# Kernel tuning notes

Measured on AMD Instinct MI355X. Metric: run time of the kernel, lower is better.

Reference implementation:

```python
import jax, jax.numpy as jnp
import numpy as np

MAX_LENGTH = 11
SOS_TOKEN = 0
H = 256      # hidden_dim
V = 32000    # output_dim (vocab)
B = 256      # batch
S = 64       # encoder seq len


def setup_inputs() -> dict:
    key = jax.random.key(0)
    ks = jax.random.split(key, 16)
    sc = 0.05
    return {
        "encoder_outputs": jax.random.normal(ks[0], (B, S, H), jnp.float32),
        "encoder_hidden": jax.random.normal(ks[1], (1, B, H), jnp.float32),
        "target_tensor": jax.random.randint(ks[2], (B, MAX_LENGTH), 0, V),
        "embedding": jax.random.normal(ks[3], (V, H), jnp.float32) * sc,
        "Wa": jax.random.normal(ks[4], (H, H), jnp.float32) * sc,
        "ba": jnp.zeros((H,), jnp.float32),
        "Ua": jax.random.normal(ks[5], (H, H), jnp.float32) * sc,
        "bua": jnp.zeros((H,), jnp.float32),
        "Va": jax.random.normal(ks[6], (H, 1), jnp.float32) * sc,
        "bva": jnp.zeros((1,), jnp.float32),
        "W_ih": jax.random.normal(ks[7], (H, 2 * H), jnp.float32) * sc,
        "b_ih": jnp.zeros((H,), jnp.float32),
        "W_hh": jax.random.normal(ks[8], (H, H), jnp.float32) * sc,
        "b_hh": jnp.zeros((H,), jnp.float32),
        "W_out": jax.random.normal(ks[9], (V, H), jnp.float32) * sc,
        "b_out": jnp.zeros((V,), jnp.float32),
    }


def _decode(encoder_outputs, encoder_hidden, target_tensor,
            embedding, Wa, ba, Ua, bua, Va, bva,
            W_ih, b_ih, W_hh, b_hh, W_out, b_out):
    batch = encoder_outputs.shape[0]
    # Ua(keys) is step-invariant: precompute once.  [B, S, H]
    uk = jnp.einsum('bsh,kh->bsk', encoder_outputs, Ua) + bua
    h0 = encoder_hidden[0]  # [B, H]
    # teacher forcing: input at step i is SOS for i=0, else target[:, i-1]
    tokens = jnp.concatenate(
        [jnp.full((batch, 1), SOS_TOKEN, dtype=target_tensor.dtype),
         target_tensor[:, :MAX_LENGTH - 1]], axis=1)  # [B, T]

    def step(h, tok):
        emb = embedding[tok]                                   # [B, H]
        q = jnp.einsum('bh,kh->bk', h, Wa) + ba                # Wa(query)
        scores = jnp.tanh(q[:, None, :] + uk) @ Va + bva       # [B, S, 1]
        attn = jax.nn.softmax(scores[..., 0], axis=-1)         # [B, S]
        ctx = jnp.einsum('bs,bsh->bh', attn, encoder_outputs)  # [B, H]
        x = jnp.concatenate([emb, ctx], axis=-1)               # [B, 2H]
        h_new = jnp.tanh(x @ W_ih.T + b_ih + h @ W_hh.T + b_hh)
        logits = h_new @ W_out.T + b_out                       # [B, V]
        return h_new, (logits, attn)

    h_last, (logits, attns) = jax.lax.scan(step, h0, tokens.T)
    decoder_outputs = jax.nn.log_softmax(
        jnp.transpose(logits, (1, 0, 2)), axis=-1)             # [B, T, V]
    attentions = jnp.transpose(attns, (1, 0, 2))               # [B, T, S]
    return decoder_outputs, h_last[None], attentions


def reference(encoder_outputs, encoder_hidden, target_tensor,
              embedding, Wa, ba, Ua, bua, Va, bva,
              W_ih, b_ih, W_hh, b_hh, W_out, b_out):
    return _decode(encoder_outputs, encoder_hidden, target_tensor,
                   embedding, Wa, ba, Ua, bua, Va, bva,
                   W_ih, b_ih, W_hh, b_hh, W_out, b_out)
```

## Files before the change

kernel.cpp:

```cpp
#include <hip/hip_runtime.h>

#define Bz 256
#define Sz 64
#define Hz 256
#define Vz 32000
#define Tz 11
#define Mz (Bz*Tz)

typedef __attribute__((ext_vector_type(8))) short bf16x8;
typedef __attribute__((ext_vector_type(4))) float f32x4;

__device__ __forceinline__ float blo(unsigned int u){ return __builtin_bit_cast(float, u<<16); }
__device__ __forceinline__ float bhi(unsigned int u){ return __builtin_bit_cast(float, u & 0xffff0000u); }
__device__ __forceinline__ unsigned short f2bf(float f){
  unsigned int x = __builtin_bit_cast(unsigned int, f);
  return (unsigned short)((x + 0x7fffu + ((x>>16)&1u)) >> 16);
}
__device__ __forceinline__ float bf2f(unsigned short u){ return __builtin_bit_cast(float, ((unsigned int)u)<<16); }
__device__ __forceinline__ float ftanh(float x){ float e = __expf(2.f*x); return 1.f - 2.f/(e+1.f); }

__device__ __forceinline__ float dot8(uint4 wv, const float* base){
  float4 h0 = *(const float4*)(base);
  float4 h1 = *(const float4*)(base+4);
  return blo(wv.x)*h0.x + bhi(wv.x)*h0.y + blo(wv.y)*h0.z + bhi(wv.y)*h0.w
       + blo(wv.z)*h1.x + bhi(wv.z)*h1.y + blo(wv.w)*h1.z + bhi(wv.w)*h1.w;
}

__device__ __forceinline__ void gll16(const unsigned short* g, unsigned short* l){
  __builtin_amdgcn_global_load_lds(
      (const __attribute__((address_space(1))) unsigned int*)g,
      (__attribute__((address_space(3))) unsigned int*)l, 16, 0, 0);
}

__global__ __launch_bounds__(256) void k_prep(
    const float* __restrict__ Wa,
    const float* __restrict__ Wih, const float* __restrict__ Whh,
    const int* __restrict__ target, const float* __restrict__ embedding,
    const float* __restrict__ b_ih,
    const float* __restrict__ enc, const float* __restrict__ Ua,
    const float* __restrict__ bua,
    unsigned short* __restrict__ wa_p,
    unsigned short* __restrict__ wih2_p, unsigned short* __restrict__ whh_p,
    float* __restrict__ E, unsigned short* __restrict__ uk_b){
  __shared__ float rows[16][Hz];
  int tid = threadIdx.x;
  int bid = blockIdx.x;
  if (bid < 256){
    int i = bid*256 + tid;
    int k = i>>8, j = i&255;
    int p = ((j>>3)*256 + k)*8 + (j&7);
    wa_p[p]   = f2bf(Wa[i]);
    whh_p[p]  = f2bf(Whh[i]);
    wih2_p[p] = f2bf(Wih[k*512 + 256 + j]);
  } else if (bid < 256+176){
    int m0 = (bid-256)*16;
    for (int r=0;r<16;r++){
      int m = m0 + r; int b = m/11, t = m - b*11;
      int tok = (t==0) ? 0 : target[b*11 + (t-1)];
      rows[r][tid] = embedding[(size_t)tok*Hz + tid];
    }
    __syncthreads();
    float acc[16];
    #pragma unroll
    for (int r=0;r<16;r++) acc[r]=0.f;
    const float* wrow = Wih + tid*512;
    for (int j4=0;j4<64;j4++){
      float4 w = *(const float4*)(wrow + j4*4);
      #pragma unroll
      for (int r=0;r<16;r++){
        float4 e = *(const float4*)(&rows[r][j4*4]);
        acc[r] += w.x*e.x + w.y*e.y + w.z*e.z + w.w*e.w;
      }
    }
    float bi = b_ih[tid];
    for (int r=0;r<16;r++) E[(m0+r)*Hz + tid] = acc[r] + bi;
  } else {
    int r0 = (bid-(256+176))*16;
    for (int r=0;r<16;r++) rows[r][tid] = enc[(size_t)(r0+r)*Hz + tid];
    __syncthreads();
    float acc[16];
    #pragma unroll
    for (int r=0;r<16;r++) acc[r]=0.f;
    const float* wrow = Ua + tid*Hz;
    for (int j4=0;j4<64;j4++){
      float4 w = *(const float4*)(wrow + j4*4);
      #pragma unroll
      for (int r=0;r<16;r++){
        float4 e = *(const float4*)(&rows[r][j4*4]);
        acc[r] += w.x*e.x + w.y*e.y + w.z*e.z + w.w*e.w;
      }
    }
    float bk = bua[tid];
    for (int r=0;r<16;r++) uk_b[(size_t)(r0+r)*Hz + tid] = f2bf(acc[r] + bk);
  }
}

__global__ __launch_bounds__(512) __attribute__((amdgpu_waves_per_eu(2,4)))
void k_rnn(
    const float* __restrict__ enc, const float* __restrict__ ench,
    const float* __restrict__ ba, const float* __restrict__ Va,
    const float* __restrict__ bva, const float* __restrict__ b_hh,
    const unsigned short* __restrict__ uk_b, const unsigned short* __restrict__ wa_p,
    const unsigned short* __restrict__ wih2_p, const unsigned short* __restrict__ whh_p,
    const float* __restrict__ E, unsigned short* __restrict__ hs_b,
    float* __restrict__ out_hlast, float* __restrict__ out_attn,
    const float* __restrict__ Wout, unsigned short* __restrict__ wout_b){
  __shared__ __align__(16) unsigned short uk_lds[Sz][Hz];
  __shared__ __align__(16) unsigned short enc_lds[Sz][Hz];
  __shared__ __align__(16) float h_lds[Hz];
  __shared__ __align__(16) float ctx_lds[Hz];
  __shared__ __align__(16) float redq[2][Hz];
  __shared__ __align__(16) float redh_a[2][Hz];
  __shared__ __align__(16) float redh[2][Hz];
  __shared__ float sc_lds[Sz];
  __shared__ float attn_lds[Sz];
  int tid = threadIdx.x;

  if (blockIdx.x >= Bz){
    int i = (blockIdx.x - Bz)*512 + tid;
    const int stride = 1024*512;
    for (int idx = i; idx < Vz*Hz; idx += stride) wout_b[idx] = f2bf(Wout[idx]);
    return;
  }

  int b = blockIdx.x;
  int k = tid & 255, qd = tid >> 8;
  int lane = tid & 63, wv = tid >> 6;
  const int rot = (b & 3) << 2;

  {
    const uint4* src = (const uint4*)(uk_b + (size_t)b*Sz*Hz);
    uint4* dst = (uint4*)(&uk_lds[0][0]);
    #pragma unroll
    for (int i=0;i<4;i++) dst[i*512+tid] = src[i*512+tid];
  }
  {
    const float4* src = (const float4*)(enc + (size_t)b*Sz*Hz);
    #pragma unroll
    for (int i=0;i<8;i++){
      int idx = i*512 + tid;
      float4 v = src[idx];
      ushort4 p; p.x=f2bf(v.x); p.y=f2bf(v.y); p.z=f2bf(v.z); p.w=f2bf(v.w);
      *(ushort4*)((unsigned short*)(&enc_lds[0][0]) + idx*4) = p;
    }
  }
  if (tid < Hz) h_lds[tid] = ench[b*Hz + tid];
  float va_r[4], ba4[4];
  #pragma unroll
  for (int c=0;c<4;c++){ va_r[c] = Va[lane + 64*c]; ba4[c] = ba[lane + 64*c]; }
  float bhh_k = b_hh[k], bva_s = bva[0];

  const uint4* wap = (const uint4*)(wa_p)   + (size_t)qd*16*256 + k;
  const uint4* whp = (const uint4*)(whh_p)  + (size_t)qd*16*256 + k;
  const uint4* w2p = (const uint4*)(wih2_p) + (size_t)qd*16*256 + k;
  __syncthreads();

  for (int t=0; t<Tz; t++){
    int m = b*Tz + t;
    const float* hb = &h_lds[qd*128];
    {
      float a0=0.f, a1=0.f, a2=0.f, a3=0.f;
      #pragma unroll 2
      for (int jx=0;jx<16;jx+=4){
        int jj = (jx + rot) & 15;
        uint4 w0=wap[(jj+0)*256], w1=wap[(jj+1)*256], w2=wap[(jj+2)*256], w3=wap[(jj+3)*256];
        a0 += dot8(w0, hb + jj*8 +  0);
        a1 += dot8(w1, hb + jj*8 +  8);
        a2 += dot8(w2, hb + jj*8 + 16);
        a3 += dot8(w3, hb + jj*8 + 24);
      }
      redq[qd][k] = (a0+a1) + (a2+a3);
      float b0=0.f, b1=0.f, b2=0.f, b3=0.f;
      #pragma unroll 2
      for (int jx=0;jx<16;jx+=4){
        int jj = (jx + rot) & 15;
        uint4 w0=whp[(jj+0)*256], w1=whp[(jj+1)*256], w2=whp[(jj+2)*256], w3=whp[(jj+3)*256];
        b0 += dot8(w0, hb + jj*8 +  0);
        b1 += dot8(w1, hb + jj*8 +  8);
        b2 += dot8(w2, hb + jj*8 + 16);
        b3 += dot8(w3, hb + jj*8 + 24);
      }
      redh_a[qd][k] = (b0+b1) + (b2+b3);
    }
    float e_pre = E[(size_t)m*Hz + k];
    __syncthreads();
    {
      float ql[4];
      #pragma unroll
      for (int c=0;c<4;c++){
        int p = lane + 64*c;
        ql[c] = redq[0][p] + redq[1][p] + ba4[c];
      }
      #pragma unroll
      for (int si=0; si<8; si++){
        int s = wv*8 + si;
        float p = 0.f;
        #pragma unroll
        for (int c=0;c<4;c++){
          float u = bf2f(uk_lds[s][lane + 64*c]);
          p += ftanh(ql[c] + u) * va_r[c];
        }
        #pragma unroll
        for (int off=1; off<64; off<<=1) p += __shfl_xor(p, off, 64);
        if (lane==0) sc_lds[s] = p + bva_s;
      }
    }
    __syncthreads();
    {
      float sv = sc_lds[lane];
      float mx = sv;
      #pragma unroll
      for (int off=1; off<64; off<<=1) mx = fmaxf(mx, __shfl_xor(mx, off, 64));
      float e = __expf(sv - mx);
      float sum = e;
      #pragma unroll
      for (int off=1; off<64; off<<=1) sum += __shfl_xor(sum, off, 64);
      float a = e / sum;
      if (wv == 0){
        attn_lds[lane] = a;
        out_attn[(size_t)m*Sz + lane] = a;
      }
    }
    __syncthreads();
    {
      float c0=0.f, c1=0.f;
      #pragma unroll
      for (int i=0;i<32;i+=2){
        int s = qd*32 + i;
        c0 += attn_lds[s]   * bf2f(enc_lds[s][k]);
        c1 += attn_lds[s+1] * bf2f(enc_lds[s+1][k]);
      }
      redq[qd][k] = c0 + c1;
    }
    __syncthreads();
    if (qd == 0) ctx_lds[k] = redq[0][k] + redq[1][k];
    __syncthreads();
    {
      const float* cb = &ctx_lds[qd*128];
      float a0=0.f, a1=0.f, a2=0.f, a3=0.f;
      #pragma unroll 2
      for (int jx=0;jx<16;jx+=4){
        int jj = (jx + rot) & 15;
        uint4 w0=w2p[(jj+0)*256], w1=w2p[(jj+1)*256], w2=w2p[(jj+2)*256], w3=w2p[(jj+3)*256];
        a0 += dot8(w0, cb + jj*8 +  0);
        a1 += dot8(w1, cb + jj*8 +  8);
        a2 += dot8(w2, cb + jj*8 + 16);
        a3 += dot8(w3, cb + jj*8 + 24);
      }
      redh[qd][k] = (a0+a1) + (a2+a3);
    }
    __syncthreads();
    if (qd == 0){
      float acc = e_pre + bhh_k
                + redh_a[0][k] + redh_a[1][k]
                + redh[0][k]   + redh[1][k];
      float hn = ftanh(acc);
      h_lds[k] = hn;
      hs_b[(size_t)m*Hz + k] = f2bf(hn);
      if (t==Tz-1) out_hlast[b*Hz + k] = hn;
    }
    __syncthreads();
  }
}

__global__ __launch_bounds__(256, 4) void k_gemm(
    const unsigned short* __restrict__ Ab, const unsigned short* __restrict__ Bb,
    const float* __restrict__ b_out, const float* __restrict__ lse,
    float* __restrict__ out, float* __restrict__ partials){
  __shared__ __align__(16) unsigned short As[128*64];
  __shared__ __align__(16) unsigned short Bs[128*64];
  int tid = threadIdx.x;
  int fid = blockIdx.x;
  int xcd = fid & 7, wu = fid >> 3;
  int wid = (xcd < 4 ? xcd*688 : 4*688 + (xcd-4)*687) + wu;
  int bn = wid / 22;
  int bm = wid - bn*22;
  int m0 = bm*128, n0 = bn*128;
  int w = tid>>6, lane = tid&63;
  int wm = w>>1, wn = w&1;
  f32x4 acc[4][4];
  #pragma unroll
  for (int i=0;i<4;i++)
    #pragma unroll
    for (int j=0;j<4;j++) acc[i][j] = (f32x4){0.f,0.f,0.f,0.f};

  for (int ktx=0; ktx<4; ktx++){
    int kt = (ktx + bm) & 3;
    __syncthreads();
    #pragma unroll
    for (int i=0;i<4;i++){
      int chunk = i*256 + tid;
      int row = chunk>>3, c8 = chunk&7;
      gll16(Ab + (size_t)(m0+row)*Hz + kt*64 + c8*8, &As[(i*256 + w*64)*8]);
      gll16(Bb + (size_t)(n0+row)*Hz + kt*64 + c8*8, &Bs[(i*256 + w*64)*8]);
    }
    __syncthreads();
    #pragma unroll
    for (int ks=0; ks<2; ks++){
      bf16x8 af[4], bg[4];
      #pragma unroll
      for (int i=0;i<4;i++){
        int row = wm*64 + i*16 + (lane&15);
        af[i] = *(const bf16x8*)(&As[row*64 + ks*32 + (lane>>4)*8]);
      }
      #pragma unroll
      for (int j=0;j<4;j++){
        int row = wn*64 + j*16 + (lane&15);
        bg[j] = *(const bf16x8*)(&Bs[row*64 + ks*32 + (lane>>4)*8]);
      }
      #pragma unroll
      for (int i=0;i<4;i++)
        #pragma unroll
        for (int j=0;j<4;j++)
          acc[i][j] = __builtin_amdgcn_mfma_f32_16x16x32_bf16(af[i], bg[j], acc[i][j], 0,0,0);
    }
  }
  int col_l = lane & 15, rgrp = lane >> 4;
  float bj[4];
  #pragma unroll
  for (int j=0;j<4;j++) bj[j] = b_out[n0 + wn*64 + j*16 + col_l];
  if (lse == nullptr){
    #pragma unroll
    for (int i=0;i<4;i++){
      int rowbase = m0 + wm*64 + i*16 + rgrp*4;
      #pragma unroll
      for (int r=0;r<4;r++){
        float se = 0.f;
        #pragma unroll
        for (int j=0;j<4;j++) se += __expf(acc[i][j][r] + bj[j]);
        se += __shfl_xor(se,1,64); se += __shfl_xor(se,2,64);
        se += __shfl_xor(se,4,64); se += __shfl_xor(se,8,64);
        if (col_l == 0) partials[(size_t)(bn*2+wn)*Mz + rowbase + r] = se;
      }
    }
  } else {
    #pragma unroll
    for (int i=0;i<4;i++){
      int rowbase = m0 + wm*64 + i*16 + rgrp*4;
      #pragma unroll
      for (int r=0;r<4;r++){
        float l = lse[rowbase + r];
        #pragma unroll
        for (int j=0;j<4;j++){
          int col = n0 + wn*64 + j*16 + col_l;
          out[(size_t)(rowbase+r)*Vz + col] = acc[i][j][r] + bj[j] - l;
        }
      }
    }
  }
}

__global__ __launch_bounds__(256) void k_lse(const float* __restrict__ partials,
                                             float* __restrict__ lse){
  int m = blockIdx.x*256 + threadIdx.x;
  if (m < Mz){
    float s = 0.f;
    for (int c=0;c<500;c++) s += partials[(size_t)c*Mz + m];
    lse[m] = logf(s);
  }
}

extern "C" void kernel_launch(void* const* d_in, const int* in_sizes, int n_in,
                              void* d_out, int out_size, void* d_ws, size_t ws_size,
                              hipStream_t stream) {
  const float* enc   = (const float*)d_in[0];
  const float* ench  = (const float*)d_in[1];
  const int*   target= (const int*)d_in[2];
  const float* emb   = (const float*)d_in[3];
  const float* Wa    = (const float*)d_in[4];
  const float* ba    = (const float*)d_in[5];
  const float* Ua    = (const float*)d_in[6];
  const float* bua   = (const float*)d_in[7];
  const float* Va    = (const float*)d_in[8];
  const float* bva   = (const float*)d_in[9];
  const float* Wih   = (const float*)d_in[10];
  const float* bih   = (const float*)d_in[11];
  const float* Whh   = (const float*)d_in[12];
  const float* bhh   = (const float*)d_in[13];
  const float* Wout  = (const float*)d_in[14];
  const float* bout  = (const float*)d_in[15];

  float* out = (float*)d_out;
  float* out_logits = out;
  float* out_hlast  = out + (size_t)Mz*Vz;
  float* out_attn   = out_hlast + Bz*Hz;

  char* ws = (char*)d_ws;
  unsigned short* wout_b = (unsigned short*)(ws);
  unsigned short* wa_p   = (unsigned short*)(ws + 16384000);
  unsigned short* wih2_p = (unsigned short*)(ws + 16515072);
  unsigned short* whh_p  = (unsigned short*)(ws + 16646144);
  unsigned short* hs_b   = (unsigned short*)(ws + 16777216);
  float*          lse    = (float*)(ws + 18219008);

  char* sc = (char*)d_out;
  unsigned short* uk_b     = (unsigned short*)(sc);
  float*          E        = (float*)(sc + 8388608);
  float*          partials = (float*)(sc + 11272192);

  k_prep <<<256+176+1024, 256, 0, stream>>>(Wa, Wih, Whh,
                                            target, emb, bih, enc, Ua, bua,
                                            wa_p, wih2_p, whh_p, E, uk_b);
  k_rnn  <<<Bz+1024, 512, 0, stream>>>(enc, ench, ba, Va, bva, bhh,
                                       uk_b, wa_p, wih2_p, whh_p, E, hs_b,
                                       out_hlast, out_attn, Wout, wout_b);
  k_gemm <<<5500, 256, 0, stream>>>(hs_b, wout_b, bout, nullptr, out_logits, partials);
  k_lse  <<<11, 256, 0, stream>>>(partials, lse);
  k_gemm <<<5500, 256, 0, stream>>>(hs_b, wout_b, bout, lse, out_logits, partials);
}
```

Baseline: 372.2 us.

## Split RNN step work across three thread groups and parallelize LSE reduction

The recurrent kernel now uses 768 threads per batch row instead of 512. The K dimension of the Wa/Whh/Wih matvecs and the context reduction are split three ways, with per-block rotation of the segment assignment, to shorten the per-step serial chain. The LSE kernel now has 8 threads cooperate per row via shuffles instead of one thread looping over 500 partials. The trade-offs are uneven segment lengths, extra reduction terms, and higher register and occupancy pressure from the larger block.

```diff
diff --git a/kernel.cpp b/kernel.cpp
--- a/kernel.cpp
+++ b/kernel.cpp
@@ -95,7 +95,7 @@
   }
 }
 
-__global__ __launch_bounds__(512) __attribute__((amdgpu_waves_per_eu(2,4)))
+__global__ __launch_bounds__(768) __attribute__((amdgpu_waves_per_eu(3,6)))
 void k_rnn(
     const float* __restrict__ enc, const float* __restrict__ ench,
     const float* __restrict__ ba, const float* __restrict__ Va,
@@ -109,16 +109,16 @@
   __shared__ __align__(16) unsigned short enc_lds[Sz][Hz];
   __shared__ __align__(16) float h_lds[Hz];
   __shared__ __align__(16) float ctx_lds[Hz];
-  __shared__ __align__(16) float redq[2][Hz];
-  __shared__ __align__(16) float redh_a[2][Hz];
-  __shared__ __align__(16) float redh[2][Hz];
+  __shared__ __align__(16) float redq[3][Hz];
+  __shared__ __align__(16) float redh_a[3][Hz];
+  __shared__ __align__(16) float redh[3][Hz];
   __shared__ float sc_lds[Sz];
   __shared__ float attn_lds[Sz];
   int tid = threadIdx.x;
 
   if (blockIdx.x >= Bz){
-    int i = (blockIdx.x - Bz)*512 + tid;
-    const int stride = 1024*512;
+    int i = (blockIdx.x - Bz)*768 + tid;
+    const int stride = 1024*768;
     for (int idx = i; idx < Vz*Hz; idx += stride) wout_b[idx] = f2bf(Wout[idx]);
     return;
   }
@@ -126,22 +126,28 @@
   int b = blockIdx.x;
   int k = tid & 255, qd = tid >> 8;
   int lane = tid & 63, wv = tid >> 6;
-  const int rot = (b & 3) << 2;
+  int qe = qd + (b % 3); if (qe >= 3) qe -= 3;
+  const int jst = (qe==0) ? 0 : (qe==1) ? 11 : 22;
+  const int jlen = (qe==2) ? 10 : 11;
+  const int dst_ = (qe==0) ? 0 : (qe==1) ? 22 : 43;
+  const int dlen = (qe==0) ? 22 : 21;
 
   {
     const uint4* src = (const uint4*)(uk_b + (size_t)b*Sz*Hz);
     uint4* dst = (uint4*)(&uk_lds[0][0]);
     #pragma unroll
-    for (int i=0;i<4;i++) dst[i*512+tid] = src[i*512+tid];
+    for (int i=0;i<3;i++){ int idx = i*768 + tid; if (idx < 2048) dst[idx] = src[idx]; }
   }
   {
     const float4* src = (const float4*)(enc + (size_t)b*Sz*Hz);
     #pragma unroll
-    for (int i=0;i<8;i++){
-      int idx = i*512 + tid;
-      float4 v = src[idx];
-      ushort4 p; p.x=f2bf(v.x); p.y=f2bf(v.y); p.z=f2bf(v.z); p.w=f2bf(v.w);
-      *(ushort4*)((unsigned short*)(&enc_lds[0][0]) + idx*4) = p;
+    for (int i=0;i<6;i++){
+      int idx = i*768 + tid;
+      if (idx < 4096){
+        float4 v = src[idx];
+        ushort4 p; p.x=f2bf(v.x); p.y=f2bf(v.y); p.z=f2bf(v.z); p.w=f2bf(v.w);
+        *(ushort4*)((unsigned short*)(&enc_lds[0][0]) + idx*4) = p;
+      }
     }
   }
   if (tid < Hz) h_lds[tid] = ench[b*Hz + tid];
@@ -150,37 +156,32 @@
   for (int c=0;c<4;c++){ va_r[c] = Va[lane + 64*c]; ba4[c] = ba[lane + 64*c]; }
   float bhh_k = b_hh[k], bva_s = bva[0];
 
-  const uint4* wap = (const uint4*)(wa_p)   + (size_t)qd*16*256 + k;
-  const uint4* whp = (const uint4*)(whh_p)  + (size_t)qd*16*256 + k;
-  const uint4* w2p = (const uint4*)(wih2_p) + (size_t)qd*16*256 + k;
+  const uint4* wap = (const uint4*)(wa_p)   + k;
+  const uint4* whp = (const uint4*)(whh_p)  + k;
+  const uint4* w2p = (const uint4*)(wih2_p) + k;
   __syncthreads();
 
   for (int t=0; t<Tz; t++){
     int m = b*Tz + t;
-    const float* hb = &h_lds[qd*128];
     {
-      float a0=0.f, a1=0.f, a2=0.f, a3=0.f;
-      #pragma unroll 2
-      for (int jx=0;jx<16;jx+=4){
-        int jj = (jx + rot) & 15;
-        uint4 w0=wap[(jj+0)*256], w1=wap[(jj+1)*256], w2=wap[(jj+2)*256], w3=wap[(jj+3)*256];
-        a0 += dot8(w0, hb + jj*8 +  0);
-        a1 += dot8(w1, hb + jj*8 +  8);
-        a2 += dot8(w2, hb + jj*8 + 16);
-        a3 += dot8(w3, hb + jj*8 + 24);
-      }
-      redq[qd][k] = (a0+a1) + (a2+a3);
-      float b0=0.f, b1=0.f, b2=0.f, b3=0.f;
-      #pragma unroll 2
-      for (int jx=0;jx<16;jx+=4){
-        int jj = (jx + rot) & 15;
-        uint4 w0=whp[(jj+0)*256], w1=whp[(jj+1)*256], w2=whp[(jj+2)*256], w3=whp[(jj+3)*256];
-        b0 += dot8(w0, hb + jj*8 +  0);
-        b1 += dot8(w1, hb + jj*8 +  8);
-        b2 += dot8(w2, hb + jj*8 + 16);
-        b3 += dot8(w3, hb + jj*8 + 24);
-      }
-      redh_a[qd][k] = (b0+b1) + (b2+b3);
+      float a0=0.f, a1=0.f;
+      for (int jx=0; jx+1<jlen; jx+=2){
+        int jj = jst + jx;
+        uint4 w0 = wap[jj*256], w1 = wap[(jj+1)*256];
+        a0 += dot8(w0, &h_lds[jj*8]);
+        a1 += dot8(w1, &h_lds[jj*8 + 8]);
+      }
+      if (jlen & 1){ int jj = jst + jlen - 1; a0 += dot8(wap[jj*256], &h_lds[jj*8]); }
+      redq[qd][k] = a0 + a1;
+      float b0=0.f, b1=0.f;
+      for (int jx=0; jx+1<jlen; jx+=2){
+        int jj = jst + jx;
+        uint4 w0 = whp[jj*256], w1 = whp[(jj+1)*256];
+        b0 += dot8(w0, &h_lds[jj*8]);
+        b1 += dot8(w1, &h_lds[jj*8 + 8]);
+      }
+      if (jlen & 1){ int jj = jst + jlen - 1; b0 += dot8(whp[jj*256], &h_lds[jj*8]); }
+      redh_a[qd][k] = b0 + b1;
     }
     float e_pre = E[(size_t)m*Hz + k];
     __syncthreads();
@@ -189,11 +190,9 @@
       #pragma unroll
       for (int c=0;c<4;c++){
         int p = lane + 64*c;
-        ql[c] = redq[0][p] + redq[1][p] + ba4[c];
-      }
-      #pragma unroll
-      for (int si=0; si<8; si++){
-        int s = wv*8 + si;
+        ql[c] = redq[0][p] + redq[1][p] + redq[2][p] + ba4[c];
+      }
+      for (int s = wv; s < Sz; s += 12){
         float p = 0.f;
         #pragma unroll
         for (int c=0;c<4;c++){
@@ -224,36 +223,33 @@
     __syncthreads();
     {
       float c0=0.f, c1=0.f;
-      #pragma unroll
-      for (int i=0;i<32;i+=2){
-        int s = qd*32 + i;
+      for (int i=0; i+1<dlen; i+=2){
+        int s = dst_ + i;
         c0 += attn_lds[s]   * bf2f(enc_lds[s][k]);
         c1 += attn_lds[s+1] * bf2f(enc_lds[s+1][k]);
       }
+      if (dlen & 1){ int s = dst_ + dlen - 1; c0 += attn_lds[s] * bf2f(enc_lds[s][k]); }
       redq[qd][k] = c0 + c1;
     }
     __syncthreads();
-    if (qd == 0) ctx_lds[k] = redq[0][k] + redq[1][k];
+    if (qd == 0) ctx_lds[k] = redq[0][k] + redq[1][k] + redq[2][k];
     __syncthreads();
     {
-      const float* cb = &ctx_lds[qd*128];
-      float a0=0.f, a1=0.f, a2=0.f, a3=0.f;
-      #pragma unroll 2
-      for (int jx=0;jx<16;jx+=4){
-        int jj = (jx + rot) & 15;
-        uint4 w0=w2p[(jj+0)*256], w1=w2p[(jj+1)*256], w2=w2p[(jj+2)*256], w3=w2p[(jj+3)*256];
-        a0 += dot8(w0, cb + jj*8 +  0);
-        a1 += dot8(w1, cb + jj*8 +  8);
-        a2 += dot8(w2, cb + jj*8 + 16);
-        a3 += dot8(w3, cb + jj*8 + 24);
-      }
-      redh[qd][k] = (a0+a1) + (a2+a3);
+      float a0=0.f, a1=0.f;
+      for (int jx=0; jx+1<jlen; jx+=2){
+        int jj = jst + jx;
+        uint4 w0 = w2p[jj*256], w1 = w2p[(jj+1)*256];
+        a0 += dot8(w0, &ctx_lds[jj*8]);
+        a1 += dot8(w1, &ctx_lds[jj*8 + 8]);
+      }
+      if (jlen & 1){ int jj = jst + jlen - 1; a0 += dot8(w2p[jj*256], &ctx_lds[jj*8]); }
+      redh[qd][k] = a0 + a1;
     }
     __syncthreads();
     if (qd == 0){
       float acc = e_pre + bhh_k
-                + redh_a[0][k] + redh_a[1][k]
-                + redh[0][k]   + redh[1][k];
+                + redh_a[0][k] + redh_a[1][k] + redh_a[2][k]
+                + redh[0][k]   + redh[1][k]   + redh[2][k];
       float hn = ftanh(acc);
       h_lds[k] = hn;
       hs_b[(size_t)m*Hz + k] = f2bf(hn);
@@ -352,12 +348,14 @@
 
 __global__ __launch_bounds__(256) void k_lse(const float* __restrict__ partials,
                                              float* __restrict__ lse){
-  int m = blockIdx.x*256 + threadIdx.x;
-  if (m < Mz){
-    float s = 0.f;
-    for (int c=0;c<500;c++) s += partials[(size_t)c*Mz + m];
-    lse[m] = logf(s);
-  }
+  int g = blockIdx.x*256 + threadIdx.x;
+  int m = g >> 3, sub = g & 7;
+  float s = 0.f;
+  for (int c = sub; c < 500; c += 8) s += partials[(size_t)c*Mz + m];
+  s += __shfl_xor(s, 1, 64);
+  s += __shfl_xor(s, 2, 64);
+  s += __shfl_xor(s, 4, 64);
+  if (sub == 0) lse[m] = logf(s);
 }
 
 extern "C" void kernel_launch(void* const* d_in, const int* in_sizes, int n_in,
@@ -401,10 +399,10 @@
   k_prep <<<256+176+1024, 256, 0, stream>>>(Wa, Wih, Whh,
                                             target, emb, bih, enc, Ua, bua,
                                             wa_p, wih2_p, whh_p, E, uk_b);
-  k_rnn  <<<Bz+1024, 512, 0, stream>>>(enc, ench, ba, Va, bva, bhh,
+  k_rnn  <<<Bz+1024, 768, 0, stream>>>(enc, ench, ba, Va, bva, bhh,
                                        uk_b, wa_p, wih2_p, whh_p, E, hs_b,
                                        out_hlast, out_attn, Wout, wout_b);
   k_gemm <<<5500, 256, 0, stream>>>(hs_b, wout_b, bout, nullptr, out_logits, partials);
-  k_lse  <<<11, 256, 0, stream>>>(partials, lse);
+  k_lse  <<<88, 256, 0, stream>>>(partials, lse);
   k_gemm <<<5500, 256, 0, stream>>>(hs_b, wout_b, bout, lse, out_logits, partials);
 }
```

Result: slower. 384.2 us (+3.2%).
